# Kernel optimization log

Hardware: AMD Instinct MI355X
Metric: run time of the kernel (lower is better)

Reference implementation:

```python
import jax, jax.numpy as jnp
import numpy as np

B, N, D, OUT = 4, 2048, 128, 64
FWD_T, REV_T = 3, 3
NEG_BIG = 1e20  # matches tf source: GRAPH*1e20 - 1e20


def setup_inputs() -> dict:
    key = jax.random.key(0)
    k = jax.random.split(key, 9)
    INPUT = jax.random.normal(k[0], (B, N, D), dtype=jnp.float32)
    # binary adjacency with ~avg degree 64 (sparsity 64/N)
    CFG = (jax.random.uniform(k[1], (B, N, N)) < 64.0 / N).astype(jnp.float32)
    LFG = jnp.zeros((B, N, N), dtype=jnp.float32)  # unused by forward (commented out in source)
    s1 = 1.0 / np.sqrt(D)
    w1 = jax.random.uniform(k[2], (D, 1), minval=-s1, maxval=s1)
    b1 = jnp.zeros((1,), jnp.float32)
    w2 = jax.random.uniform(k[3], (D, 1), minval=-s1, maxval=s1)
    b2 = jnp.zeros((1,), jnp.float32)
    W = jax.random.uniform(k[4], (D, D), minval=-s1, maxval=s1)  # weightDense, no bias
    Wout = jax.random.uniform(k[5], (D, OUT), minval=-s1, maxval=s1)
    bout = jnp.zeros((OUT,), jnp.float32)
    return {"INPUT": INPUT, "CFG": CFG, "LFG": LFG, "w1": w1, "b1": b1,
            "w2": w2, "b2": b2, "W": W, "Wout": Wout, "bout": bout}


def _attention(x, g, w1, b1, w2, b2):
    # x: [B,N,D], g: [B,N,N] binary adjacency
    ah1 = x @ w1 + b1                      # [B,N,1]
    ah2 = x @ w2 + b2                      # [B,N,1]
    eij = ah1 + jnp.transpose(ah2, (0, 2, 1))   # [B,N,N]
    e_graph = g * NEG_BIG - NEG_BIG        # 0 where edge, -1e20 where no edge
    return jax.nn.softmax(jax.nn.leaky_relu(eij, negative_slope=0.2) + e_graph, axis=-1)


def _propagate(x, g, n_iter, w1, b1, w2, b2, W):
    for _ in range(n_iter):
        a = _attention(x, g, w1, b1, w2, b2) * g      # re-mask after softmax
        trans = jnp.einsum('bij,bjd->bid', a, x @ W)  # graph matmul (dropout off: eval mode)
        x = jax.nn.elu(x + trans)
    return x


def reference(INPUT, CFG, LFG, w1, b1, w2, b2, W, Wout, bout):
    fwd = _propagate(jax.nn.relu(INPUT), CFG, FWD_T, w1, b1, w2, b2, W)
    rev = _propagate(jax.nn.relu(INPUT), jnp.transpose(CFG, (0, 2, 1)), REV_T, w1, b1, w2, b2, W)
    mid = jnp.sum(fwd + rev, axis=1)       # [B,D]
    return mid @ Wout + bout               # [B,OUT]
```

## Files before the change

kernel.cpp:

```cpp
#include <hip/hip_runtime.h>
#include <hip/hip_fp16.h>
#include <cstdint>
#include <cstddef>

#define Bn 4
#define Nn 2048
#define Dn 128
#define OUTn 64
#define Sn 8
#define MAXDEG 128
#define NITER 3

typedef _Float16 half8 __attribute__((ext_vector_type(8)));
typedef float floatx4 __attribute__((ext_vector_type(4)));

__device__ __forceinline__ unsigned long long spread4(unsigned long long x) {
    x &= 0xFFFFull;
    x = (x | (x << 24)) & 0x000000FF000000FFull;
    x = (x | (x << 12)) & 0x000F000F000F000Full;
    x = (x | (x << 6))  & 0x0303030303030303ull;
    x = (x | (x << 3))  & 0x1111111111111111ull;
    return x;
}

__global__ void fwd_bits_init(const float4* __restrict__ cfg4,
                              unsigned long long* __restrict__ bits,
                              int* __restrict__ adj, int* __restrict__ deg,
                              const float4* __restrict__ in4, float4* __restrict__ x4,
                              __half* __restrict__ xh,
                              const float* __restrict__ W, __half* __restrict__ WhT,
                              const float* __restrict__ w1, const float* __restrict__ b1,
                              const float* __restrict__ w2, const float* __restrict__ b2,
                              float* __restrict__ ah1, float* __restrict__ ah2) {
    if (blockIdx.x >= (Bn * Nn) / 4 + (Bn * Nn) / 8) {
        int t = threadIdx.x;
        if (t < Dn) {
            for (int k = 0; k < Dn; ++k)
                WhT[(size_t)t * Dn + k] = __float2half(W[(size_t)k * Dn + t]);
        }
        return;
    }
    if (blockIdx.x >= (Bn * Nn) / 4) {
        int blk = blockIdx.x - (Bn * Nn) / 4;
        int t = threadIdx.x;
        int row = blk * 8 + (t >> 5);
        int q   = t & 31;
        float4 v = in4[(size_t)row * 32 + q];
        v.x = v.x > 0.f ? v.x : 0.f;
        v.y = v.y > 0.f ? v.y : 0.f;
        v.z = v.z > 0.f ? v.z : 0.f;
        v.w = v.w > 0.f ? v.w : 0.f;
        x4[(size_t)row * 32 + q] = v;
        x4[(size_t)(Bn * Nn * Dn) / 4 + (size_t)row * 32 + q] = v;
        __half2 p0h = __floats2half2_rn(v.x, v.y);
        __half2 p1h = __floats2half2_rn(v.z, v.w);
        uint2 u2;
        u2.x = *(unsigned*)&p0h; u2.y = *(unsigned*)&p1h;
        ((uint2*)xh)[(size_t)row * 32 + q] = u2;
        ((uint2*)xh)[(size_t)(Bn * Nn) * 32 + (size_t)row * 32 + q] = u2;
        const float4* w14 = (const float4*)w1;
        const float4* w24 = (const float4*)w2;
        float4 wa = w14[q], wb = w24[q];
        float p1 = v.x * wa.x + v.y * wa.y + v.z * wa.z + v.w * wa.w;
        float p2 = v.x * wb.x + v.y * wb.y + v.z * wb.z + v.w * wb.w;
        #pragma unroll
        for (int o = 16; o >= 1; o >>= 1) {
            p1 += __shfl_xor(p1, o);
            p2 += __shfl_xor(p2, o);
        }
        if (q == 0) {
            float a1 = p1 + b1[0], a2 = p2 + b2[0];
            ah1[row] = a1; ah1[Bn * Nn + row] = a1;
            ah2[row] = a2; ah2[Bn * Nn + row] = a2;
        }
        return;
    }
    int row  = blockIdx.x * 4 + (threadIdx.x >> 6);
    int lane = threadIdx.x & 63;
    int b = row >> 11;
    int i = row & (Nn - 1);
    const float4* crow = cfg4 + (size_t)row * (Nn / 4);
    int* dst = adj + (size_t)row * MAXDEG;
    int cnt = 0;
    for (int j0 = 0; j0 < Nn; j0 += 256) {
        float4 v = crow[(j0 >> 2) + lane];
        int nib = (v.x != 0.f) | ((v.y != 0.f) << 1) |
                  ((v.z != 0.f) << 2) | ((v.w != 0.f) << 3);
        unsigned long long m0 = __ballot(nib & 1);
        unsigned long long m1 = __ballot(nib & 2);
        unsigned long long m2 = __ballot(nib & 4);
        unsigned long long m3 = __ballot(nib & 8);
        unsigned long long below = (1ull << lane) - 1ull;
        int off = __popcll(m0 & below) + __popcll(m1 & below) +
                  __popcll(m2 & below) + __popcll(m3 & below);
        int total = __popcll(m0) + __popcll(m1) + __popcll(m2) + __popcll(m3);
        int base = cnt + off;
        int col = j0 + 4 * lane;
        if (nib & 1) { if (base < MAXDEG) dst[base] = col;     base++; }
        if (nib & 2) { if (base < MAXDEG) dst[base] = col + 1; base++; }
        if (nib & 4) { if (base < MAXDEG) dst[base] = col + 2; base++; }
        if (nib & 8) { if (base < MAXDEG) dst[base] = col + 3; base++; }
        if (lane < 4) {
            int sh = lane << 4;
            unsigned long long w = spread4(m0 >> sh) | (spread4(m1 >> sh) << 1) |
                                   (spread4(m2 >> sh) << 2) | (spread4(m3 >> sh) << 3);
            int jw = (j0 >> 6) + lane;
            bits[((size_t)(b * 32 + jw)) * Nn + i] = w;
        }
        cnt += total;
    }
    if (lane == 0) deg[row] = (cnt < MAXDEG ? cnt : MAXDEG);
}

__device__ __forceinline__ void gemm_tile_mfma(const __half* __restrict__ xh,
                                               const __half* __restrict__ WhT,
                                               __half* __restrict__ xwh, int tile) {
    int lane = threadIdx.x & 63;
    int rowTile = tile >> 3, colTile = tile & 7;
    int mn = lane & 15, kseg = lane >> 4;
    const uint4* Arow = (const uint4*)(xh + ((size_t)(rowTile * 16 + mn)) * Dn);
    const uint4* Brow = (const uint4*)(WhT + ((size_t)(colTile * 16 + mn)) * Dn);
    floatx4 c = {0.f, 0.f, 0.f, 0.f};
    #pragma unroll
    for (int ks = 0; ks < 4; ++ks) {
        uint4 au = Arow[ks * 4 + kseg];
        uint4 bu = Brow[ks * 4 + kseg];
        half8 a = *(half8*)&au;
        half8 b = *(half8*)&bu;
        c = __builtin_amdgcn_mfma_f32_16x16x32_f16(a, b, c, 0, 0, 0);
    }
    int row = (lane >> 4) * 4;
    __half* dst = xwh + ((size_t)(rowTile * 16 + row)) * Dn + colTile * 16 + mn;
    #pragma unroll
    for (int rg = 0; rg < 4; ++rg)
        dst[(size_t)rg * Dn] = __float2half(c[rg]);
}

__global__ void gemm_rev(const __half* __restrict__ xh, const __half* __restrict__ WhT,
                         __half* __restrict__ xwh,
                         const unsigned long long* __restrict__ bits,
                         int* __restrict__ adj, int* __restrict__ deg) {
    if (blockIdx.x < 2048) {
        gemm_tile_mfma(xh, WhT, xwh, blockIdx.x * 4 + (threadIdx.x >> 6));
        return;
    }
    int r    = (blockIdx.x - 2048) * 4 + (threadIdx.x >> 6);
    int lane = threadIdx.x & 63;
    int b = r >> 11;
    int j = r & (Nn - 1);
    const unsigned long long* col = bits + ((size_t)(b * 32 + (j >> 6))) * Nn;
    int bit = j & 63;
    int out_r = (Bn + b) * Nn + j;
    int* dst = adj + (size_t)out_r * MAXDEG;
    int cnt = 0;
    for (int i0 = 0; i0 < Nn; i0 += 64) {
        unsigned long long word = col[i0 + lane];
        bool e = (word >> bit) & 1;
        unsigned long long m = __ballot(e);
        if (e) {
            int pos = cnt + __popcll(m & ((1ull << lane) - 1ull));
            if (pos < MAXDEG) dst[pos] = i0 + lane;
        }
        cnt += __popcll(m);
    }
    if (lane == 0) deg[out_r] = (cnt < MAXDEG ? cnt : MAXDEG);
}

__global__ void gemm_mfma(const __half* __restrict__ xh, const __half* __restrict__ WhT,
                          __half* __restrict__ xwh) {
    gemm_tile_mfma(xh, WhT, xwh, blockIdx.x * 4 + (threadIdx.x >> 6));
}

__global__ __launch_bounds__(256) void attn_agg(
        float* __restrict__ x, __half* __restrict__ xh,
        const __half* __restrict__ xwh,
        const int* __restrict__ adj, const int* __restrict__ deg,
        const float* __restrict__ ah1r, const float* __restrict__ ah2r,
        float* __restrict__ ah1w, float* __restrict__ ah2w,
        const float* __restrict__ gw1, const float* __restrict__ gb1,
        const float* __restrict__ gw2, const float* __restrict__ gb2) {
    int w    = threadIdx.x >> 6;
    int lane = threadIdx.x & 63;
    int s = blockIdx.x & 7;
    int i = (blockIdx.x >> 3) * 4 + w;
    int r = s * Nn + i;

    __shared__ float2 pn[4][MAXDEG];

    int d = deg[r]; if (d > MAXDEG) d = MAXDEG;

    float a1 = ah1r[r];
    const int* al = adj + (size_t)r * MAXDEG;
    const float* ah2s = ah2r + (size_t)s * Nn;
    int jlo = 0, jhi = 0;
    float elo = -INFINITY, ehi = -INFINITY;
    if (lane < d) {
        jlo = al[lane];
        float e = a1 + ah2s[jlo];
        elo = e > 0.f ? e : 0.2f * e;
    }
    if (lane + 64 < d) {
        jhi = al[lane + 64];
        float e = a1 + ah2s[jhi];
        ehi = e > 0.f ? e : 0.2f * e;
    }
    float m = fmaxf(elo, ehi);
    #pragma unroll
    for (int o = 32; o > 0; o >>= 1) m = fmaxf(m, __shfl_xor(m, o));
    float exlo = (lane < d)      ? __expf(elo - m) : 0.f;
    float exhi = (lane + 64 < d) ? __expf(ehi - m) : 0.f;
    float sum = exlo + exhi;
    #pragma unroll
    for (int o = 32; o > 0; o >>= 1) sum += __shfl_xor(sum, o);
    float inv = (d > 0) ? 1.0f / sum : 0.f;

    pn[w][lane]      = make_float2(exlo, __int_as_float(jlo));
    pn[w][lane + 64] = make_float2(exhi, __int_as_float(jhi));

    const uint4* xwu = (const uint4*)(xwh + (size_t)s * Nn * Dn);
    int g = lane >> 4;
    int f = lane & 15;
    __half2 acc2[4];
    #pragma unroll
    for (int e = 0; e < 4; ++e) acc2[e] = __halves2half2(__float2half(0.f), __float2half(0.f));
    int dpad = (d + 15) & ~15;
    for (int base = 0; base < dpad; base += 16) {
        float2 q[4];
        uint4  v[4];
        #pragma unroll
        for (int t = 0; t < 4; ++t) q[t] = pn[w][base + 4 * t + g];
        #pragma unroll
        for (int t = 0; t < 4; ++t)
            v[t] = xwu[(size_t)__float_as_int(q[t].y) * 16 + f];
        #pragma unroll
        for (int t = 0; t < 4; ++t) {
            __half   ph = __float2half(q[t].x);
            __half2  p2 = __halves2half2(ph, ph);
            const __half2* hh = (const __half2*)&v[t];
            acc2[0] = __hfma2(p2, hh[0], acc2[0]);
            acc2[1] = __hfma2(p2, hh[1], acc2[1]);
            acc2[2] = __hfma2(p2, hh[2], acc2[2]);
            acc2[3] = __hfma2(p2, hh[3], acc2[3]);
        }
    }
    float2 f0 = __half22float2(acc2[0]);
    float2 f1 = __half22float2(acc2[1]);
    float2 f2 = __half22float2(acc2[2]);
    float2 f3 = __half22float2(acc2[3]);
    float accA[4] = { f0.x, f0.y, f1.x, f1.y };
    float accB[4] = { f2.x, f2.y, f3.x, f3.y };
    #pragma unroll
    for (int e = 0; e < 4; ++e) {
        accA[e] += __shfl_xor(accA[e], 16);
        accA[e] += __shfl_xor(accA[e], 32);
        accB[e] += __shfl_xor(accB[e], 16);
        accB[e] += __shfl_xor(accB[e], 32);
    }

    if (lane < 16) {
        float4* x4 = (float4*)(x + (size_t)r * Dn);
        float4 vA4 = x4[2 * lane], vB4 = x4[2 * lane + 1];
        float4 tA, tB, rA, rB;
        tA.x = vA4.x + accA[0] * inv;  tA.y = vA4.y + accA[1] * inv;
        tA.z = vA4.z + accA[2] * inv;  tA.w = vA4.w + accA[3] * inv;
        tB.x = vB4.x + accB[0] * inv;  tB.y = vB4.y + accB[1] * inv;
        tB.z = vB4.z + accB[2] * inv;  tB.w = vB4.w + accB[3] * inv;
        rA.x = tA.x > 0.f ? tA.x : (expf(tA.x) - 1.f);
        rA.y = tA.y > 0.f ? tA.y : (expf(tA.y) - 1.f);
        rA.z = tA.z > 0.f ? tA.z : (expf(tA.z) - 1.f);
        rA.w = tA.w > 0.f ? tA.w : (expf(tA.w) - 1.f);
        rB.x = tB.x > 0.f ? tB.x : (expf(tB.x) - 1.f);
        rB.y = tB.y > 0.f ? tB.y : (expf(tB.y) - 1.f);
        rB.z = tB.z > 0.f ? tB.z : (expf(tB.z) - 1.f);
        rB.w = tB.w > 0.f ? tB.w : (expf(tB.w) - 1.f);
        x4[2 * lane]     = rA;
        x4[2 * lane + 1] = rB;

        __half2 h0 = __floats2half2_rn(rA.x, rA.y);
        __half2 h1 = __floats2half2_rn(rA.z, rA.w);
        __half2 h2 = __floats2half2_rn(rB.x, rB.y);
        __half2 h3 = __floats2half2_rn(rB.z, rB.w);
        uint4 u;
        u.x = *(unsigned*)&h0; u.y = *(unsigned*)&h1;
        u.z = *(unsigned*)&h2; u.w = *(unsigned*)&h3;
        ((uint4*)(xh + (size_t)r * Dn))[lane] = u;

        const float4* w14 = (const float4*)gw1;
        const float4* w24 = (const float4*)gw2;
        float4 wa = w14[2 * lane], wb = w14[2 * lane + 1];
        float4 ua = w24[2 * lane], ub = w24[2 * lane + 1];
        float p1 = rA.x * wa.x + rA.y * wa.y + rA.z * wa.z + rA.w * wa.w
                 + rB.x * wb.x + rB.y * wb.y + rB.z * wb.z + rB.w * wb.w;
        float p2 = rA.x * ua.x + rA.y * ua.y + rA.z * ua.z + rA.w * ua.w
                 + rB.x * ub.x + rB.y * ub.y + rB.z * ub.z + rB.w * ub.w;
        #pragma unroll
        for (int o = 8; o >= 1; o >>= 1) {
            p1 += __shfl_xor(p1, o);
            p2 += __shfl_xor(p2, o);
        }
        if (lane == 0) {
            ah1w[r] = p1 + gb1[0];
            ah2w[r] = p2 + gb2[0];
        }
    }
}

__global__ void reduce_partial(const float* __restrict__ x, float* __restrict__ part) {
    int b = blockIdx.x >> 5;
    int c = blockIdx.x & 31;
    int tid = threadIdx.x;
    const float* xf = x + ((size_t)(b * Nn) + c * 64) * Dn;
    const float* xr = x + ((size_t)((4 + b) * Nn) + c * 64) * Dn;
    float sv = 0.f;
    for (int i = 0; i < 64; ++i)
        sv += xf[(size_t)i * Dn + tid] + xr[(size_t)i * Dn + tid];
    part[(size_t)blockIdx.x * Dn + tid] = sv;
}

__global__ void final_out(const float* __restrict__ part,
                          const float* __restrict__ Wout, const float* __restrict__ bout,
                          float* __restrict__ out) {
    int b = blockIdx.x;
    int tid = threadIdx.x;
    __shared__ float mid[Dn];
    float sv = 0.f;
    for (int c = 0; c < 32; ++c) sv += part[(size_t)(b * 32 + c) * Dn + tid];
    mid[tid] = sv;
    __syncthreads();
    if (tid < OUTn) {
        float o = bout[tid];
        #pragma unroll 4
        for (int k = 0; k < Dn; ++k) o = fmaf(mid[k], Wout[k * OUTn + tid], o);
        out[b * OUTn + tid] = o;
    }
}

extern "C" void kernel_launch(void* const* d_in, const int* in_sizes, int n_in,
                              void* d_out, int out_size, void* d_ws, size_t ws_size,
                              hipStream_t stream) {
    const float* INPUT = (const float*)d_in[0];
    const float* CFG   = (const float*)d_in[1];
    const float* w1    = (const float*)d_in[3];
    const float* b1    = (const float*)d_in[4];
    const float* w2    = (const float*)d_in[5];
    const float* b2    = (const float*)d_in[6];
    const float* Wm    = (const float*)d_in[7];
    const float* Wout  = (const float*)d_in[8];
    const float* bout  = (const float*)d_in[9];
    float* out = (float*)d_out;

    float*  x    = (float*)d_ws;
    __half* xwh  = (__half*)(x + (size_t)Sn * Nn * Dn);
    __half* xh   = xwh + (size_t)Sn * Nn * Dn;
    __half* WhT  = xh + (size_t)Sn * Nn * Dn;
    int*    adj  = (int*)(WhT + (size_t)Dn * Dn);
    int*    deg  = adj + (size_t)Sn * Nn * MAXDEG;
    float*  ah1a = (float*)(deg + Sn * Nn);
    float*  ah2a = ah1a + Sn * Nn;
    float*  ah1b = ah2a + Sn * Nn;
    float*  ah2b = ah1b + Sn * Nn;
    float*  part = ah2b + Sn * Nn;
    unsigned long long* bits = (unsigned long long*)(part + Bn * 32 * Dn);

    fwd_bits_init<<<(Bn * Nn) / 4 + (Bn * Nn) / 8 + 1, 256, 0, stream>>>(
        (const float4*)CFG, bits, adj, deg, (const float4*)INPUT, (float4*)x,
        xh, Wm, WhT, w1, b1, w2, b2, ah1a, ah2a);

    for (int it = 0; it < NITER; ++it) {
        if (it == 0) {
            gemm_rev<<<4096, 256, 0, stream>>>(xh, WhT, xwh, bits, adj, deg);
        } else {
            gemm_mfma<<<2048, 256, 0, stream>>>(xh, WhT, xwh);
        }
        const float* r1 = (it & 1) ? ah1b : ah1a;
        const float* r2 = (it & 1) ? ah2b : ah2a;
        float* w1p = (it & 1) ? ah1a : ah1b;
        float* w2p = (it & 1) ? ah2a : ah2b;
        attn_agg<<<(Sn * Nn) / 4, 256, 0, stream>>>(
            x, xh, xwh, adj, deg, r1, r2, w1p, w2p, w1, b1, w2, b2);
    }

    reduce_partial<<<Bn * 32, 128, 0, stream>>>(x, part);
    final_out     <<<Bn, 128, 0, stream>>>(part, Wout, bout, out);
}
```

Before: 141.0 us.

## Reassociate graph matmul to aggregate x first, then multiply by W inside attention kernel

```diff
diff --git a/kernel.cpp b/kernel.cpp
--- a/kernel.cpp
+++ b/kernel.cpp
@@ -10,9 +10,6 @@
 #define Sn 8
 #define MAXDEG 128
 #define NITER 3
-
-typedef _Float16 half8 __attribute__((ext_vector_type(8)));
-typedef float floatx4 __attribute__((ext_vector_type(4)));
 
 __device__ __forceinline__ unsigned long long spread4(unsigned long long x) {
     x &= 0xFFFFull;
@@ -112,39 +109,9 @@
     if (lane == 0) deg[row] = (cnt < MAXDEG ? cnt : MAXDEG);
 }
 
-__device__ __forceinline__ void gemm_tile_mfma(const __half* __restrict__ xh,
-                                               const __half* __restrict__ WhT,
-                                               __half* __restrict__ xwh, int tile) {
-    int lane = threadIdx.x & 63;
-    int rowTile = tile >> 3, colTile = tile & 7;
-    int mn = lane & 15, kseg = lane >> 4;
-    const uint4* Arow = (const uint4*)(xh + ((size_t)(rowTile * 16 + mn)) * Dn);
-    const uint4* Brow = (const uint4*)(WhT + ((size_t)(colTile * 16 + mn)) * Dn);
-    floatx4 c = {0.f, 0.f, 0.f, 0.f};
-    #pragma unroll
-    for (int ks = 0; ks < 4; ++ks) {
-        uint4 au = Arow[ks * 4 + kseg];
-        uint4 bu = Brow[ks * 4 + kseg];
-        half8 a = *(half8*)&au;
-        half8 b = *(half8*)&bu;
-        c = __builtin_amdgcn_mfma_f32_16x16x32_f16(a, b, c, 0, 0, 0);
-    }
-    int row = (lane >> 4) * 4;
-    __half* dst = xwh + ((size_t)(rowTile * 16 + row)) * Dn + colTile * 16 + mn;
-    #pragma unroll
-    for (int rg = 0; rg < 4; ++rg)
-        dst[(size_t)rg * Dn] = __float2half(c[rg]);
-}
-
-__global__ void gemm_rev(const __half* __restrict__ xh, const __half* __restrict__ WhT,
-                         __half* __restrict__ xwh,
-                         const unsigned long long* __restrict__ bits,
-                         int* __restrict__ adj, int* __restrict__ deg) {
-    if (blockIdx.x < 2048) {
-        gemm_tile_mfma(xh, WhT, xwh, blockIdx.x * 4 + (threadIdx.x >> 6));
-        return;
-    }
-    int r    = (blockIdx.x - 2048) * 4 + (threadIdx.x >> 6);
+__global__ void rev_adj(const unsigned long long* __restrict__ bits,
+                        int* __restrict__ adj, int* __restrict__ deg) {
+    int r    = blockIdx.x * 4 + (threadIdx.x >> 6);
     int lane = threadIdx.x & 63;
     int b = r >> 11;
     int j = r & (Nn - 1);
@@ -166,17 +133,13 @@
     if (lane == 0) deg[out_r] = (cnt < MAXDEG ? cnt : MAXDEG);
 }
 
-__global__ void gemm_mfma(const __half* __restrict__ xh, const __half* __restrict__ WhT,
-                          __half* __restrict__ xwh) {
-    gemm_tile_mfma(xh, WhT, xwh, blockIdx.x * 4 + (threadIdx.x >> 6));
-}
-
-__global__ __launch_bounds__(256) void attn_agg(
-        float* __restrict__ x, __half* __restrict__ xh,
-        const __half* __restrict__ xwh,
+__global__ __launch_bounds__(256) void attn_fused(
+        float* __restrict__ x,
+        const __half* __restrict__ xh_r, __half* __restrict__ xh_w,
         const int* __restrict__ adj, const int* __restrict__ deg,
         const float* __restrict__ ah1r, const float* __restrict__ ah2r,
         float* __restrict__ ah1w, float* __restrict__ ah2w,
+        const __half* __restrict__ WhT,
         const float* __restrict__ gw1, const float* __restrict__ gb1,
         const float* __restrict__ gw2, const float* __restrict__ gb2) {
     int w    = threadIdx.x >> 6;
@@ -185,7 +148,8 @@
     int i = (blockIdx.x >> 3) * 4 + w;
     int r = s * Nn + i;
 
-    __shared__ float2 pn[4][MAXDEG];
+    __shared__ float2   pn[4][MAXDEG];
+    __shared__ unsigned aggLds[4][64];
 
     int d = deg[r]; if (d > MAXDEG) d = MAXDEG;
 
@@ -217,7 +181,7 @@
     pn[w][lane]      = make_float2(exlo, __int_as_float(jlo));
     pn[w][lane + 64] = make_float2(exhi, __int_as_float(jhi));
 
-    const uint4* xwu = (const uint4*)(xwh + (size_t)s * Nn * Dn);
+    const uint4* xhu = (const uint4*)(xh_r + (size_t)s * Nn * Dn);
     int g = lane >> 4;
     int f = lane & 15;
     __half2 acc2[4];
@@ -231,7 +195,7 @@
         for (int t = 0; t < 4; ++t) q[t] = pn[w][base + 4 * t + g];
         #pragma unroll
         for (int t = 0; t < 4; ++t)
-            v[t] = xwu[(size_t)__float_as_int(q[t].y) * 16 + f];
+            v[t] = xhu[(size_t)__float_as_int(q[t].y) * 16 + f];
         #pragma unroll
         for (int t = 0; t < 4; ++t) {
             __half   ph = __float2half(q[t].x);
@@ -258,50 +222,57 @@
     }
 
     if (lane < 16) {
-        float4* x4 = (float4*)(x + (size_t)r * Dn);
-        float4 vA4 = x4[2 * lane], vB4 = x4[2 * lane + 1];
-        float4 tA, tB, rA, rB;
-        tA.x = vA4.x + accA[0] * inv;  tA.y = vA4.y + accA[1] * inv;
-        tA.z = vA4.z + accA[2] * inv;  tA.w = vA4.w + accA[3] * inv;
-        tB.x = vB4.x + accB[0] * inv;  tB.y = vB4.y + accB[1] * inv;
-        tB.z = vB4.z + accB[2] * inv;  tB.w = vB4.w + accB[3] * inv;
-        rA.x = tA.x > 0.f ? tA.x : (expf(tA.x) - 1.f);
-        rA.y = tA.y > 0.f ? tA.y : (expf(tA.y) - 1.f);
-        rA.z = tA.z > 0.f ? tA.z : (expf(tA.z) - 1.f);
-        rA.w = tA.w > 0.f ? tA.w : (expf(tA.w) - 1.f);
-        rB.x = tB.x > 0.f ? tB.x : (expf(tB.x) - 1.f);
-        rB.y = tB.y > 0.f ? tB.y : (expf(tB.y) - 1.f);
-        rB.z = tB.z > 0.f ? tB.z : (expf(tB.z) - 1.f);
-        rB.w = tB.w > 0.f ? tB.w : (expf(tB.w) - 1.f);
-        x4[2 * lane]     = rA;
-        x4[2 * lane + 1] = rB;
-
-        __half2 h0 = __floats2half2_rn(rA.x, rA.y);
-        __half2 h1 = __floats2half2_rn(rA.z, rA.w);
-        __half2 h2 = __floats2half2_rn(rB.x, rB.y);
-        __half2 h3 = __floats2half2_rn(rB.z, rB.w);
-        uint4 u;
-        u.x = *(unsigned*)&h0; u.y = *(unsigned*)&h1;
-        u.z = *(unsigned*)&h2; u.w = *(unsigned*)&h3;
-        ((uint4*)(xh + (size_t)r * Dn))[lane] = u;
-
-        const float4* w14 = (const float4*)gw1;
-        const float4* w24 = (const float4*)gw2;
-        float4 wa = w14[2 * lane], wb = w14[2 * lane + 1];
-        float4 ua = w24[2 * lane], ub = w24[2 * lane + 1];
-        float p1 = rA.x * wa.x + rA.y * wa.y + rA.z * wa.z + rA.w * wa.w
-                 + rB.x * wb.x + rB.y * wb.y + rB.z * wb.z + rB.w * wb.w;
-        float p2 = rA.x * ua.x + rA.y * ua.y + rA.z * ua.z + rA.w * ua.w
-                 + rB.x * ub.x + rB.y * ub.y + rB.z * ub.z + rB.w * ub.w;
-        #pragma unroll
-        for (int o = 8; o >= 1; o >>= 1) {
-            p1 += __shfl_xor(p1, o);
-            p2 += __shfl_xor(p2, o);
-        }
-        if (lane == 0) {
-            ah1w[r] = p1 + gb1[0];
-            ah2w[r] = p2 + gb2[0];
-        }
+        __half2 m0 = __floats2half2_rn(accA[0] * inv, accA[1] * inv);
+        __half2 m1 = __floats2half2_rn(accA[2] * inv, accA[3] * inv);
+        __half2 m2 = __floats2half2_rn(accB[0] * inv, accB[1] * inv);
+        __half2 m3 = __floats2half2_rn(accB[2] * inv, accB[3] * inv);
+        aggLds[w][4 * lane + 0] = *(unsigned*)&m0;
+        aggLds[w][4 * lane + 1] = *(unsigned*)&m1;
+        aggLds[w][4 * lane + 2] = *(unsigned*)&m2;
+        aggLds[w][4 * lane + 3] = *(unsigned*)&m3;
+    }
+
+    const uint4* wr0 = (const uint4*)(WhT + (size_t)lane * Dn);
+    const uint4* wr1 = (const uint4*)(WhT + (size_t)(lane + 64) * Dn);
+    __half2 t0 = __halves2half2(__float2half(0.f), __float2half(0.f));
+    __half2 t1 = t0;
+    #pragma unroll 4
+    for (int ch = 0; ch < 16; ++ch) {
+        uint4 u0 = wr0[ch];
+        uint4 u1 = wr1[ch];
+        #pragma unroll
+        for (int q = 0; q < 4; ++q) {
+            unsigned au = aggLds[w][4 * ch + q];
+            __half2 a2 = *(__half2*)&au;
+            t0 = __hfma2(a2, ((const __half2*)&u0)[q], t0);
+            t1 = __hfma2(a2, ((const __half2*)&u1)[q], t1);
+        }
+    }
+    float tr0 = __half2float(__low2half(t0)) + __half2float(__high2half(t0));
+    float tr1 = __half2float(__low2half(t1)) + __half2float(__high2half(t1));
+
+    size_t xbase = (size_t)r * Dn;
+    float v0 = x[xbase + lane];
+    float v1 = x[xbase + lane + 64];
+    float s0 = v0 + tr0;
+    float s1 = v1 + tr1;
+    s0 = s0 > 0.f ? s0 : (expf(s0) - 1.f);
+    s1 = s1 > 0.f ? s1 : (expf(s1) - 1.f);
+    x[xbase + lane]      = s0;
+    x[xbase + lane + 64] = s1;
+    xh_w[xbase + lane]      = __float2half(s0);
+    xh_w[xbase + lane + 64] = __float2half(s1);
+
+    float p1 = s0 * gw1[lane] + s1 * gw1[lane + 64];
+    float p2 = s0 * gw2[lane] + s1 * gw2[lane + 64];
+    #pragma unroll
+    for (int o = 32; o > 0; o >>= 1) {
+        p1 += __shfl_xor(p1, o);
+        p2 += __shfl_xor(p2, o);
+    }
+    if (lane == 0) {
+        ah1w[r] = p1 + gb1[0];
+        ah2w[r] = p2 + gb2[0];
     }
 }
 
@@ -350,9 +321,9 @@
     float* out = (float*)d_out;
 
     float*  x    = (float*)d_ws;
-    __half* xwh  = (__half*)(x + (size_t)Sn * Nn * Dn);
-    __half* xh   = xwh + (size_t)Sn * Nn * Dn;
-    __half* WhT  = xh + (size_t)Sn * Nn * Dn;
+    __half* xh_a = (__half*)(x + (size_t)Sn * Nn * Dn);
+    __half* xh_b = xh_a + (size_t)Sn * Nn * Dn;
+    __half* WhT  = xh_b + (size_t)Sn * Nn * Dn;
     int*    adj  = (int*)(WhT + (size_t)Dn * Dn);
     int*    deg  = adj + (size_t)Sn * Nn * MAXDEG;
     float*  ah1a = (float*)(deg + Sn * Nn);
@@ -364,20 +335,18 @@
 
     fwd_bits_init<<<(Bn * Nn) / 4 + (Bn * Nn) / 8 + 1, 256, 0, stream>>>(
         (const float4*)CFG, bits, adj, deg, (const float4*)INPUT, (float4*)x,
-        xh, Wm, WhT, w1, b1, w2, b2, ah1a, ah2a);
+        xh_a, Wm, WhT, w1, b1, w2, b2, ah1a, ah2a);
+    rev_adj<<<(Bn * Nn) / 4, 256, 0, stream>>>(bits, adj, deg);
 
     for (int it = 0; it < NITER; ++it) {
-        if (it == 0) {
-            gemm_rev<<<4096, 256, 0, stream>>>(xh, WhT, xwh, bits, adj, deg);
-        } else {
-            gemm_mfma<<<2048, 256, 0, stream>>>(xh, WhT, xwh);
-        }
+        const __half* xr = (it & 1) ? xh_b : xh_a;
+        __half*       xw = (it & 1) ? xh_a : xh_b;
         const float* r1 = (it & 1) ? ah1b : ah1a;
         const float* r2 = (it & 1) ? ah2b : ah2a;
         float* w1p = (it & 1) ? ah1a : ah1b;
         float* w2p = (it & 1) ? ah2a : ah2b;
-        attn_agg<<<(Sn * Nn) / 4, 256, 0, stream>>>(
-            x, xh, xwh, adj, deg, r1, r2, w1p, w2p, w1, b1, w2, b2);
+        attn_fused<<<(Sn * Nn) / 4, 256, 0, stream>>>(
+            x, xr, xw, adj, deg, r1, r2, w1p, w2p, WhT, w1, b1, w2, b2);
     }
 
     reduce_partial<<<Bn * 32, 128, 0, stream>>>(x, part);
```

Result: slower. 274.1 us (+94.3%).
